# Performance work log

Hardware: AMD Instinct MI355X
Metric: run time of the kernel (lower is better)

The kernel has to match this reference:

```python
import jax, jax.numpy as jnp
import numpy as np

# __init__ defaults of BoxSelector
NMS_T = 0.5
TOP_K = 400
CONF_T = 0.5
KEEP_K = 200
# standard SSD BoxCoder variances
V0, V1 = 0.1, 0.2
BIG = 1e9
B, N, C = 128, 32768, 6  # batch, num_priors, 4 loc + 2 classes


def decode(loc, priors):
    # SSD decode: priors are (cx, cy, w, h); returns (x1, y1, x2, y2)
    cxcy = priors[:, :2] + loc[:, :2] * V0 * priors[:, 2:]
    wh = priors[:, 2:] * jnp.exp(loc[:, 2:] * V1)
    return jnp.concatenate([cxcy - wh * 0.5, cxcy + wh * 0.5], axis=1)


def pairwise_iou(b):
    # b: [K, 4] xyxy -> [K, K] IoU
    x1, y1, x2, y2 = b[:, 0], b[:, 1], b[:, 2], b[:, 3]
    area = (x2 - x1) * (y2 - y1)
    iw = jnp.clip(jnp.minimum(x2[:, None], x2[None, :]) - jnp.maximum(x1[:, None], x1[None, :]), 0.0)
    ih = jnp.clip(jnp.minimum(y2[:, None], y2[None, :]) - jnp.maximum(y1[:, None], y1[None, :]), 0.0)
    inter = iw * ih
    return inter / (area[:, None] + area[None, :] - inter + 1e-12)


def _select_image(pred, priorboxes):
    loc, confs = pred[:, :4], pred[:, 4:]
    boxes = decode(loc, priorboxes)                       # [N, 4]
    scores = jnp.max(confs, axis=1)                       # [N]
    labels = jnp.argmax(confs, axis=1)                    # [N] int
    # confidence filter (mask instead of dynamic gather, jit-friendly)
    masked = jnp.where(scores > CONF_T, scores, -BIG)
    top_s, idx = jax.lax.top_k(masked, TOP_K)             # descending, [K]
    cand_boxes = boxes[idx]                               # [K, 4]
    cand_labels = labels[idx]                             # [K]
    valid = top_s > CONF_T                                # padding from filter
    # greedy NMS over the top_k candidates (already score-sorted desc)
    iou = pairwise_iou(cand_boxes)                        # [K, K]
    j = jnp.arange(TOP_K)
    def body(i, keep):
        sup = keep[i] & (iou[i] > NMS_T) & (j > i)
        return keep & ~sup
    keep = jax.lax.fori_loop(0, TOP_K, body, valid)
    # original sorts kept scores ASCENDING and takes the first keep_top_k
    sort_key = jnp.where(keep, top_s, BIG)                # invalid sort last
    order = jnp.argsort(sort_key)[:KEEP_K]                # [keep_top_k]
    out = jnp.concatenate(
        [cand_labels[order, None].astype(jnp.float32),
         top_s[order, None],
         cand_boxes[order]], axis=1)                      # [keep_top_k, 6]
    return jnp.where(keep[order][:, None], out, 0.0)


def setup_inputs() -> dict:
    key = jax.random.key(0)
    k1, k2 = jax.random.split(key)
    predictions = jax.random.normal(k1, (B, N, C), dtype=jnp.float32)
    priors = jax.random.uniform(k2, (N, 4), dtype=jnp.float32)
    return {"predictions": predictions, "priors": priors}


def reference(predictions, priors):
    priorboxes = priors[:, :4]
    return jax.vmap(lambda p: _select_image(p, priorboxes))(predictions)  # [B, keep_top_k, 6]
```

## Files before the change

kernel.cpp:

```cpp
#include <hip/hip_runtime.h>
#include <stdint.h>

#define BB 128
#define NN 32768
#define CI 6
#define TOPK 400
#define KEEPK 200
#define SORTN 1024
#define NT 1024
#define KQT 8
#define NBUCK 4096
#define KEY0 0x3F000000u

#define IOU_C 0.50000002980232238769531250

__global__ __launch_bounds__(256) void score_kernel(
        const float* __restrict__ pred, uint32_t* __restrict__ keys) {
    int g = blockIdx.x * 256 + threadIdx.x;
    const float4* p4 = reinterpret_cast<const float4*>(pred) + (size_t)g * 3;
    float4 b = p4[1];
    float4 c = p4[2];
    float s0 = fmaxf(b.x, b.y);
    float s1 = fmaxf(c.z, c.w);
    uint2 o;
    o.x = (s0 > 0.5f) ? __float_as_uint(s0) : 0u;
    o.y = (s1 > 0.5f) ? __float_as_uint(s1) : 0u;
    *reinterpret_cast<uint2*>(keys + (size_t)g * 2) = o;
}

__global__ __launch_bounds__(NT) void boxsel2_kernel(
        const float* __restrict__ pred, const float* __restrict__ priors,
        const uint32_t* __restrict__ keys, float* __restrict__ out) {
    const int b = blockIdx.x;
    const int tid = threadIdx.x;
    const int lane = tid & 63;
    const int wid = tid >> 6;
    const float* img = pred + (size_t)b * (NN * CI);
    float* oimg = out + (size_t)b * KEEPK * 6;

    __shared__ union {
        unsigned int hist[2][NBUCK];
        struct {
            unsigned long long cbuf[SORTN];
            unsigned long long cbuf2[SORTN];
            float4 cbox[TOPK];
            float car[TOPK], csc[TOPK];
            int clab[TOPK];
            unsigned long long supm[TOPK * 7 + 8];
        } s;
    } u;
    __shared__ unsigned int wavetot[16];
    __shared__ unsigned int sh_bucket, sh_above, ccount;
    __shared__ unsigned long long keepw[8];

    for (int i = tid; i < KEEPK * 6; i += NT) oimg[i] = 0.0f;

    uint4 kq[KQT];
    const uint4* k4 = reinterpret_cast<const uint4*>(keys + (size_t)b * NN);
#pragma unroll
    for (int uu = 0; uu < KQT; uu++) kq[uu] = k4[tid + (uu << 10)];

    if (tid == 0) { sh_bucket = 0; sh_above = 0; ccount = 0; }
    if (tid < 8) keepw[tid] = 0ull;
    for (int i = tid; i < 2 * NBUCK; i += NT) ((unsigned int*)u.hist)[i] = 0u;
    __syncthreads();

    const int hc = wid & 1;
#pragma unroll
    for (int uu = 0; uu < KQT; uu++) {
        uint32_t k0 = kq[uu].x, k1 = kq[uu].y, k2 = kq[uu].z, k3 = kq[uu].w;
        if (k0) { unsigned int bu = (k0 - KEY0) >> 13; if (bu > NBUCK - 1u) bu = NBUCK - 1u; atomicAdd(&u.hist[hc][bu], 1u); }
        if (k1) { unsigned int bu = (k1 - KEY0) >> 13; if (bu > NBUCK - 1u) bu = NBUCK - 1u; atomicAdd(&u.hist[hc][bu], 1u); }
        if (k2) { unsigned int bu = (k2 - KEY0) >> 13; if (bu > NBUCK - 1u) bu = NBUCK - 1u; atomicAdd(&u.hist[hc][bu], 1u); }
        if (k3) { unsigned int bu = (k3 - KEY0) >> 13; if (bu > NBUCK - 1u) bu = NBUCK - 1u; atomicAdd(&u.hist[hc][bu], 1u); }
    }
    __syncthreads();

    unsigned int h0 = u.hist[0][4 * tid + 0] + u.hist[1][4 * tid + 0];
    unsigned int h1 = u.hist[0][4 * tid + 1] + u.hist[1][4 * tid + 1];
    unsigned int h2 = u.hist[0][4 * tid + 2] + u.hist[1][4 * tid + 2];
    unsigned int h3 = u.hist[0][4 * tid + 3] + u.hist[1][4 * tid + 3];
    unsigned int sum = h0 + h1 + h2 + h3;
    unsigned int suf = sum;
#pragma unroll
    for (int off = 1; off < 64; off <<= 1) {
        unsigned int v = __shfl_down(suf, off);
        if (lane + off < 64) suf += v;
    }
    if (lane == 0) wavetot[wid] = suf;
    __syncthreads();
    if (tid < 16) {
        unsigned int wv = wavetot[tid];
        unsigned int ws = wv;
#pragma unroll
        for (int off = 1; off < 16; off <<= 1) {
            unsigned int v = __shfl_down(ws, off);
            if (tid + off < 16) ws += v;
        }
        wavetot[tid] = ws - wv;
    }
    __syncthreads();
    unsigned int acc = wavetot[wid] + (suf - sum);
    if (acc < TOPK && acc + h3 >= TOPK) { sh_bucket = 4 * tid + 3; sh_above = acc; }
    acc += h3;
    if (acc < TOPK && acc + h2 >= TOPK) { sh_bucket = 4 * tid + 2; sh_above = acc; }
    acc += h2;
    if (acc < TOPK && acc + h1 >= TOPK) { sh_bucket = 4 * tid + 1; sh_above = acc; }
    acc += h1;
    if (acc < TOPK && acc + h0 >= TOPK) { sh_bucket = 4 * tid + 0; sh_above = acc; }
    __syncthreads();
    const unsigned int B = sh_bucket;

    u.s.cbuf2[tid] = 0ull;
    __syncthreads();
#pragma unroll
    for (int uu = 0; uu < KQT; uu++) {
        uint32_t kk[4] = { kq[uu].x, kq[uu].y, kq[uu].z, kq[uu].w };
#pragma unroll
        for (int j = 0; j < 4; j++) {
            uint32_t key = kk[j];
            if (key != 0u) {
                unsigned int bu = (key - KEY0) >> 13;
                if (bu > NBUCK - 1u) bu = NBUCK - 1u;
                if (bu >= B) {
                    unsigned int p = atomicAdd(&ccount, 1u);
                    if (p < SORTN) {
                        unsigned int idx = ((unsigned int)(tid + (uu << 10)) << 2) + (unsigned int)j;
                        u.s.cbuf[p] = ((unsigned long long)key << 32) |
                                      (unsigned long long)(0xFFFFFFFFu - idx);
                    }
                }
            }
        }
    }
    __syncthreads();

    {
        const unsigned int cnt = (ccount < SORTN) ? ccount : SORTN;
        if ((unsigned int)tid < cnt) {
            unsigned long long ct = u.s.cbuf[tid];
            unsigned int rank = 0;
#pragma unroll 4
            for (unsigned int j = 0; j < cnt; j++)
                rank += (u.s.cbuf[j] > ct) ? 1u : 0u;
            u.s.cbuf2[rank] = ct;
        }
    }
    __syncthreads();

    if (tid < TOPK) {
        const int t = tid;
        unsigned long long c = u.s.cbuf2[t];
        uint32_t key = (uint32_t)(c >> 32);
        uint32_t idx = 0xFFFFFFFFu - (uint32_t)(c & 0xFFFFFFFFull);
        int valid = (key != 0u) && (idx < NN);
        float x1 = 0.f, y1 = 0.f, x2 = 0.f, y2 = 0.f;
        int lab = 0;
        if (valid) {
            const float* p = img + (size_t)idx * CI;
            float l0 = p[0], l1 = p[1], l2 = p[2], l3 = p[3], c0 = p[4], c1 = p[5];
            const float* pr = priors + (size_t)idx * 4;
            float px = pr[0], py = pr[1], pw = pr[2], ph = pr[3];
            float cxv = __fadd_rn(px, __fmul_rn(__fmul_rn(l0, 0.1f), pw));
            float cyv = __fadd_rn(py, __fmul_rn(__fmul_rn(l1, 0.1f), ph));
            float ew = __fmul_rn(pw, expf(__fmul_rn(l2, 0.2f)));
            float eh = __fmul_rn(ph, expf(__fmul_rn(l3, 0.2f)));
            float hw = __fmul_rn(ew, 0.5f);
            float hh = __fmul_rn(eh, 0.5f);
            x1 = __fsub_rn(cxv, hw); y1 = __fsub_rn(cyv, hh);
            x2 = __fadd_rn(cxv, hw); y2 = __fadd_rn(cyv, hh);
            lab = (c1 > c0) ? 1 : 0;
        }
        u.s.cbox[t] = make_float4(x1, y1, x2, y2);
        u.s.csc[t] = __uint_as_float(key);
        u.s.car[t] = __fmul_rn(__fsub_rn(x2, x1), __fsub_rn(y2, y1));
        u.s.clab[t] = lab;
        if (valid) atomicOr(&keepw[t >> 6], 1ull << (t & 63));
    }
    __syncthreads();

    for (int task = tid; task < TOPK * 7; task += NT) {
        int i = task / 7;
        int w4 = task - i * 7;
        int jbase = w4 << 6;
        int jmax = (TOPK - jbase < 64) ? (TOPK - jbase) : 64;
        int j0 = i + 1 - jbase; if (j0 < 0) j0 = 0;
        unsigned long long word = 0ull;
        if (j0 < jmax) {
            float4 bi = u.s.cbox[i]; float ai = u.s.car[i];
            for (int jj = j0; jj < jmax; jj++) {
                int j = jbase + jj;
                float4 bj = u.s.cbox[j]; float aj = u.s.car[j];
                float iw = fmaxf(__fsub_rn(fminf(bi.z, bj.z), fmaxf(bi.x, bj.x)), 0.0f);
                float ih = fmaxf(__fsub_rn(fminf(bi.w, bj.w), fmaxf(bi.y, bj.y)), 0.0f);
                float inter = __fmul_rn(iw, ih);
                float denom = __fadd_rn(__fsub_rn(__fadd_rn(ai, aj), inter), 1e-12f);
                if ((double)inter > (double)denom * IOU_C) word |= (1ull << jj);
            }
        }
        u.s.supm[i * 7 + w4] = word;
    }
    __syncthreads();

    if (tid < 64) {
        int w = tid & 7;
        unsigned long long kw = keepw[w];
        unsigned long long rr[16], nn[16];
#pragma unroll
        for (int k = 0; k < 16; k++) rr[k] = u.s.supm[k * 7 + w];
        for (int base = 0; base < TOPK; base += 16) {
            int nb = base + 16;
            int gb = (nb < TOPK) ? nb : base;
#pragma unroll
            for (int k = 0; k < 16; k++) nn[k] = u.s.supm[(gb + k) * 7 + w];
#pragma unroll
            for (int k = 0; k < 16; k++) {
                int i = base + k;
                unsigned long long wv = __shfl(kw, i >> 6);
                if ((wv >> (i & 63)) & 1ull) kw &= ~rr[k];
            }
#pragma unroll
            for (int k = 0; k < 16; k++) rr[k] = nn[k];
        }
        if (tid < 7) keepw[tid] = kw;
    }
    __syncthreads();

    if (tid < TOPK) {
        const int t = tid;
        if ((keepw[t >> 6] >> (t & 63)) & 1ull) {
            float st = u.s.csc[t];
            int rank = 0;
#pragma unroll
            for (int w = 0; w < 7; w++) {
                unsigned long long kws = keepw[w];
                int jb = w << 6;
                unsigned long long m;
                if (t >= jb + 63)      m = 0ull;
                else if (t < jb)       m = ~0ull;
                else                   m = ~((1ull << (t - jb + 1)) - 1ull);
                rank += __popcll(kws & m);
            }
            for (int j = t + 1; j < TOPK && u.s.csc[j] == st; j++)
                if ((keepw[j >> 6] >> (j & 63)) & 1ull) rank--;
            for (int j = t - 1; j >= 0 && u.s.csc[j] == st; j--)
                if ((keepw[j >> 6] >> (j & 63)) & 1ull) rank++;
            if (rank < KEEPK) {
                float4 bx = u.s.cbox[t];
                float* row = oimg + (size_t)rank * 6;
                row[0] = (float)u.s.clab[t];
                row[1] = st;
                row[2] = bx.x; row[3] = bx.y; row[4] = bx.z; row[5] = bx.w;
            }
        }
    }
}

extern "C" void kernel_launch(void* const* d_in, const int* in_sizes, int n_in,
                              void* d_out, int out_size, void* d_ws, size_t ws_size,
                              hipStream_t stream) {
    const float* pred = (const float*)d_in[0];
    const float* priors = (const float*)d_in[1];
    float* out = (float*)d_out;
    uint32_t* keys = (uint32_t*)d_ws;
    score_kernel<<<(BB * NN / 2) / 256, 256, 0, stream>>>(pred, keys);
    boxsel2_kernel<<<BB, NT, 0, stream>>>(pred, priors, keys, out);
}
```

Before: 219.1 us.

## Build NMS suppression bitmask with wave ballots and simplify candidate threshold test

The IoU suppression matrix is now computed with one candidate row per wave and one column per lane, and each 64-bit mask word is formed by a wave ballot. This replaces the per-thread serial inner loop over up to 64 columns, which had divergent trip counts. Column boxes are held in registers across rows, and the supm array is zeroed first because lower-triangle words are now skipped. The bucket comparison for candidate gathering becomes a single key threshold compare, and the score kernel also loads the unused first float4 of each row, apparently to produce fuller contiguous memory accesses.

New measurement: 204.9 us. 1.07x faster.

```diff
diff --git a/kernel.cpp b/kernel.cpp
--- a/kernel.cpp
+++ b/kernel.cpp
@@ -18,8 +18,10 @@
         const float* __restrict__ pred, uint32_t* __restrict__ keys) {
     int g = blockIdx.x * 256 + threadIdx.x;
     const float4* p4 = reinterpret_cast<const float4*>(pred) + (size_t)g * 3;
+    float4 a = p4[0];
     float4 b = p4[1];
     float4 c = p4[2];
+    asm volatile("" :: "v"(a.x));
     float s0 = fmaxf(b.x, b.y);
     float s1 = fmaxf(c.z, c.w);
     uint2 o;
@@ -50,7 +52,7 @@
         } s;
     } u;
     __shared__ unsigned int wavetot[16];
-    __shared__ unsigned int sh_bucket, sh_above, ccount;
+    __shared__ unsigned int sh_bucket, ccount;
     __shared__ unsigned long long keepw[8];
 
     for (int i = tid; i < KEEPK * 6; i += NT) oimg[i] = 0.0f;
@@ -60,7 +62,7 @@
 #pragma unroll
     for (int uu = 0; uu < KQT; uu++) kq[uu] = k4[tid + (uu << 10)];
 
-    if (tid == 0) { sh_bucket = 0; sh_above = 0; ccount = 0; }
+    if (tid == 0) { sh_bucket = 0; ccount = 0; }
     if (tid < 8) keepw[tid] = 0ull;
     for (int i = tid; i < 2 * NBUCK; i += NT) ((unsigned int*)u.hist)[i] = 0u;
     __syncthreads();
@@ -101,15 +103,15 @@
     }
     __syncthreads();
     unsigned int acc = wavetot[wid] + (suf - sum);
-    if (acc < TOPK && acc + h3 >= TOPK) { sh_bucket = 4 * tid + 3; sh_above = acc; }
+    if (acc < TOPK && acc + h3 >= TOPK) sh_bucket = 4 * tid + 3;
     acc += h3;
-    if (acc < TOPK && acc + h2 >= TOPK) { sh_bucket = 4 * tid + 2; sh_above = acc; }
+    if (acc < TOPK && acc + h2 >= TOPK) sh_bucket = 4 * tid + 2;
     acc += h2;
-    if (acc < TOPK && acc + h1 >= TOPK) { sh_bucket = 4 * tid + 1; sh_above = acc; }
+    if (acc < TOPK && acc + h1 >= TOPK) sh_bucket = 4 * tid + 1;
     acc += h1;
-    if (acc < TOPK && acc + h0 >= TOPK) { sh_bucket = 4 * tid + 0; sh_above = acc; }
-    __syncthreads();
-    const unsigned int B = sh_bucket;
+    if (acc < TOPK && acc + h0 >= TOPK) sh_bucket = 4 * tid + 0;
+    __syncthreads();
+    const uint32_t Tkey = KEY0 + (sh_bucket << 13);
 
     u.s.cbuf2[tid] = 0ull;
     __syncthreads();
@@ -119,16 +121,12 @@
 #pragma unroll
         for (int j = 0; j < 4; j++) {
             uint32_t key = kk[j];
-            if (key != 0u) {
-                unsigned int bu = (key - KEY0) >> 13;
-                if (bu > NBUCK - 1u) bu = NBUCK - 1u;
-                if (bu >= B) {
-                    unsigned int p = atomicAdd(&ccount, 1u);
-                    if (p < SORTN) {
-                        unsigned int idx = ((unsigned int)(tid + (uu << 10)) << 2) + (unsigned int)j;
-                        u.s.cbuf[p] = ((unsigned long long)key << 32) |
-                                      (unsigned long long)(0xFFFFFFFFu - idx);
-                    }
+            if (key >= Tkey) {
+                unsigned int p = atomicAdd(&ccount, 1u);
+                if (p < SORTN) {
+                    unsigned int idx = ((unsigned int)(tid + (uu << 10)) << 2) + (unsigned int)j;
+                    u.s.cbuf[p] = ((unsigned long long)key << 32) |
+                                  (unsigned long long)(0xFFFFFFFFu - idx);
                 }
             }
         }
@@ -148,6 +146,7 @@
     }
     __syncthreads();
 
+    for (int i2 = tid; i2 < TOPK * 7 + 8; i2 += NT) u.s.supm[i2] = 0ull;
     if (tid < TOPK) {
         const int t = tid;
         unsigned long long c = u.s.cbuf2[t];
@@ -179,26 +178,34 @@
     }
     __syncthreads();
 
-    for (int task = tid; task < TOPK * 7; task += NT) {
-        int i = task / 7;
-        int w4 = task - i * 7;
-        int jbase = w4 << 6;
-        int jmax = (TOPK - jbase < 64) ? (TOPK - jbase) : 64;
-        int j0 = i + 1 - jbase; if (j0 < 0) j0 = 0;
-        unsigned long long word = 0ull;
-        if (j0 < jmax) {
-            float4 bi = u.s.cbox[i]; float ai = u.s.car[i];
-            for (int jj = j0; jj < jmax; jj++) {
-                int j = jbase + jj;
-                float4 bj = u.s.cbox[j]; float aj = u.s.car[j];
+    {
+        float4 bjv[7]; float ajv[7];
+#pragma unroll
+        for (int jw = 0; jw < 7; jw++) {
+            int j = (jw << 6) + lane;
+            int jc = (j < TOPK) ? j : (TOPK - 1);
+            bjv[jw] = u.s.cbox[jc];
+            ajv[jw] = u.s.car[jc];
+        }
+        for (int i = wid; i < TOPK; i += 16) {
+            float4 bi = u.s.cbox[i];
+            float ai = u.s.car[i];
+            const int jw0 = i >> 6;
+#pragma unroll
+            for (int jw = 0; jw < 7; jw++) {
+                if (jw < jw0) continue;
+                int j = (jw << 6) + lane;
+                float4 bj = bjv[jw]; float aj = ajv[jw];
                 float iw = fmaxf(__fsub_rn(fminf(bi.z, bj.z), fmaxf(bi.x, bj.x)), 0.0f);
                 float ih = fmaxf(__fsub_rn(fminf(bi.w, bj.w), fmaxf(bi.y, bj.y)), 0.0f);
                 float inter = __fmul_rn(iw, ih);
                 float denom = __fadd_rn(__fsub_rn(__fadd_rn(ai, aj), inter), 1e-12f);
-                if ((double)inter > (double)denom * IOU_C) word |= (1ull << jj);
-            }
-        }
-        u.s.supm[i * 7 + w4] = word;
+                bool bit = (j > i) && (j < TOPK) &&
+                           ((double)inter > (double)denom * IOU_C);
+                unsigned long long word = __ballot(bit);
+                if (lane == 0) u.s.supm[i * 7 + jw] = word;
+            }
+        }
     }
     __syncthreads();
 
```
